# Optimization experiments

Measured on AMD Instinct MI355X. Metric: run time of the kernel, lower is better.

The kernel has to match this reference:

```python
import jax, jax.numpy as jnp
import numpy as np

D_MODEL = 1024
NUM_HEADS = 16
HEAD_DIM = D_MODEL // NUM_HEADS
SCALE = HEAD_DIM ** -0.5


def setup_inputs() -> dict:
    key = jax.random.key(0)
    ks = jax.random.split(key, 5)
    x = jax.random.normal(ks[0], (2, 2048, D_MODEL), dtype=jnp.float32)
    w_qkv = jax.random.normal(ks[1], (D_MODEL, 3 * D_MODEL), dtype=jnp.float32) * (D_MODEL ** -0.5)
    b_qkv = jnp.zeros((3 * D_MODEL,), dtype=jnp.float32)
    w_out = jax.random.normal(ks[2], (D_MODEL, D_MODEL), dtype=jnp.float32) * (D_MODEL ** -0.5)
    b_out = jnp.zeros((D_MODEL,), dtype=jnp.float32)
    return {"x": x, "w_qkv": w_qkv, "b_qkv": b_qkv, "w_out": w_out, "b_out": b_out}


def reference(x, w_qkv, b_qkv, w_out, b_out):
    b, t, _ = x.shape
    qkv = x @ w_qkv + b_qkv  # [b, t, 3*d_model]
    q, k, v = jnp.split(qkv, 3, axis=-1)
    # b t (h d) -> b h t d
    def heads(z):
        return z.reshape(b, t, NUM_HEADS, HEAD_DIM).transpose(0, 2, 1, 3)
    q, k, v = heads(q), heads(k), heads(v)
    scores = jnp.einsum('bhtd,bhsd->bhts', q, k) * SCALE
    causal = jnp.tril(jnp.ones((t, t), dtype=bool))  # True = keep
    scores = jnp.where(causal, scores, -jnp.inf)
    weights = jax.nn.softmax(scores, axis=-1)
    out = jnp.einsum('bhts,bhsd->bhtd', weights, v)
    out = out.transpose(0, 2, 1, 3).reshape(b, t, D_MODEL)  # b h t d -> b t (h d)
    return out @ w_out + b_out
```

## Files before the change

kernel.cpp:

```cpp
#include <hip/hip_runtime.h>

#define D_MODEL 1024
#define NHEADS 16
#define HDIM 64
#define SEQ 2048
#define BATCH 2
#define M_TOTAL (BATCH * SEQ)
#define N_QKV (3 * D_MODEL)

typedef __attribute__((ext_vector_type(8))) short short8;
typedef __attribute__((ext_vector_type(4))) float f32x4;
typedef __attribute__((ext_vector_type(4))) unsigned short u16x4;
typedef unsigned short u16;

__device__ __forceinline__ u16 f2bf(float f) {
  union { float f; unsigned u; } v; v.f = f;
  unsigned u = v.u + 0x7fffu + ((v.u >> 16) & 1u);
  return (u16)(u >> 16);
}

__device__ __forceinline__ unsigned pack_bf16(float lo, float hi) {
  return (unsigned)f2bf(lo) | ((unsigned)f2bf(hi) << 16);
}

__device__ __forceinline__ void gload_lds16(const void* g, void* l) {
  __builtin_amdgcn_global_load_lds(
      (__attribute__((address_space(1))) void*)(g),
      (__attribute__((address_space(3))) void*)(l),
      16, 0, 0);
}

__global__ void k_cvt_bf16(const float* __restrict__ src, u16* __restrict__ dst, int n4) {
  int i = blockIdx.x * blockDim.x + threadIdx.x;
  if (i >= n4) return;
  const float4 v = reinterpret_cast<const float4*>(src)[i];
  u16x4 o;
  o.x = f2bf(v.x); o.y = f2bf(v.y); o.z = f2bf(v.z); o.w = f2bf(v.w);
  reinterpret_cast<u16x4*>(dst)[i] = o;
}

__global__ void k_transpose_bf16(const float* __restrict__ src, u16* __restrict__ dst, int R, int C) {
  __shared__ float tile[32][33];
  const int bx = blockIdx.x * 32;
  const int by = blockIdx.y * 32;
  const int tx = threadIdx.x, ty = threadIdx.y;
  #pragma unroll
  for (int i = ty; i < 32; i += 8) tile[i][tx] = src[(size_t)(by + i) * C + bx + tx];
  __syncthreads();
  #pragma unroll
  for (int i = ty; i < 32; i += 8) dst[(size_t)(bx + i) * R + by + tx] = f2bf(tile[tx][i]);
}

template <int K, int BM, int BN, int WC>
__device__ __forceinline__ void gemm_core(const u16* __restrict__ A, const u16* __restrict__ Bt,
                                          int m0, int n0, u16* As, u16* Bs, f32x4* acc) {
  constexpr int WR = 4 / WC;
  constexpr int MI = BM / WR / 16;
  constexpr int NI = BN / WC / 16;
  const int tid = threadIdx.x;
  const int lane = tid & 63;
  const int lr = lane & 15, lg = lane >> 4;
  const int wid = tid >> 6;
  const int wr = (wid / WC) * (BM / WR);
  const int wc = (wid % WC) * (BN / WC);
  for (int kt = 0; kt < K; kt += 32) {
    #pragma unroll
    for (int r = 0; r < BM / 64; ++r) {
      const int off = r * 4096 + tid * 16;
      const int row = off >> 6, colb = off & 63;
      gload_lds16((const char*)A + ((size_t)(m0 + row) * K + kt) * 2 + colb, (char*)As + off);
    }
    #pragma unroll
    for (int r = 0; r < BN / 64; ++r) {
      const int off = r * 4096 + tid * 16;
      const int row = off >> 6, colb = off & 63;
      gload_lds16((const char*)Bt + ((size_t)(n0 + row) * K + kt) * 2 + colb, (char*)Bs + off);
    }
    __syncthreads();
    short8 a[MI], b[NI];
    #pragma unroll
    for (int i = 0; i < MI; ++i) a[i] = *(const short8*)&As[(wr + i * 16 + lr) * 32 + lg * 8];
    #pragma unroll
    for (int i = 0; i < NI; ++i) b[i] = *(const short8*)&Bs[(wc + i * 16 + lr) * 32 + lg * 8];
    #pragma unroll
    for (int mi = 0; mi < MI; ++mi)
      #pragma unroll
      for (int ni = 0; ni < NI; ++ni)
        acc[mi * NI + ni] = __builtin_amdgcn_mfma_f32_16x16x32_bf16(a[mi], b[ni], acc[mi * NI + ni], 0, 0, 0);
    __syncthreads();
  }
}

__global__ __launch_bounds__(256) void k_gemm_qkv(const u16* __restrict__ A, const u16* __restrict__ Bt,
                                                  const float* __restrict__ bias,
                                                  u16* __restrict__ qb, u16* __restrict__ kb,
                                                  u16* __restrict__ vb) {
  __shared__ u16 As[128 * 32];
  __shared__ u16 Bs[128 * 32];
  f32x4 acc[16] = {};
  const int m0 = blockIdx.x * 128, n0 = blockIdx.y * 128;
  gemm_core<D_MODEL, 128, 128, 2>(A, Bt, m0, n0, As, Bs, acc);
  const int lane = threadIdx.x & 63, lr = lane & 15, lg = lane >> 4;
  const int wid = threadIdx.x >> 6;
  const int wr = (wid >> 1) * 64, wc = (wid & 1) * 64;
  #pragma unroll
  for (int ni = 0; ni < 4; ++ni) {
    const int col = n0 + wc + ni * 16 + lr;
    const float bv = bias[col];
    const int which = col >> 10;
    const int h = (col >> 6) & 15;
    const int d = col & 63;
    #pragma unroll
    for (int mi = 0; mi < 4; ++mi) {
      #pragma unroll
      for (int j = 0; j < 4; ++j) {
        const int rw = m0 + wr + mi * 16 + lg * 4 + j;
        const int bb = rw >> 11, t = rw & (SEQ - 1);
        const u16 val = f2bf(acc[mi * 4 + ni][j] + bv);
        const int bh = bb * NHEADS + h;
        if (which == 0)      qb[((size_t)bh * SEQ + t) * HDIM + d] = val;
        else if (which == 1) kb[((size_t)bh * SEQ + t) * HDIM + d] = val;
        else                 vb[((size_t)bh * HDIM + d) * SEQ + t] = val;
      }
    }
  }
}

__global__ __launch_bounds__(256) void k_gemm_out(const u16* __restrict__ A, const u16* __restrict__ Bt,
                                                  const float* __restrict__ bias,
                                                  float* __restrict__ out) {
  __shared__ u16 As[64 * 32];
  __shared__ u16 Bs[128 * 32];
  f32x4 acc[8] = {};
  const int m0 = blockIdx.x * 64, n0 = blockIdx.y * 128;
  gemm_core<D_MODEL, 64, 128, 4>(A, Bt, m0, n0, As, Bs, acc);
  const int lane = threadIdx.x & 63, lr = lane & 15, lg = lane >> 4;
  const int wid = threadIdx.x >> 6;
  const int wc = wid * 32;
  #pragma unroll
  for (int ni = 0; ni < 2; ++ni) {
    const int col = n0 + wc + ni * 16 + lr;
    const float bv = bias[col];
    #pragma unroll
    for (int mi = 0; mi < 4; ++mi) {
      #pragma unroll
      for (int j = 0; j < 4; ++j) {
        const int rw = m0 + mi * 16 + lg * 4 + j;
        out[(size_t)rw * D_MODEL + col] = acc[mi * 2 + ni][j] + bv;
      }
    }
  }
}

__global__ __launch_bounds__(256) void k_attn(const u16* __restrict__ qb, const u16* __restrict__ kb,
                                              const u16* __restrict__ vb, u16* __restrict__ attn) {
  __shared__ u16 Ks[2][64 * 64];
  __shared__ u16 Vs[2][64 * 64];
  __shared__ u16 Pl[4][16 * 64];
  const int tid = threadIdx.x, lane = tid & 63, wid = tid >> 6;
  const int lr = lane & 15, lg = lane >> 4;
  const int lin = blockIdx.x;
  const int r = lin >> 8, c = lin & 255;
  const int a = c >> 3;
  const int qrank = (r & 1) ? a : (31 - a);
  const int bh = (c & 7) | (r << 3);
  const int b = bh >> 4, h = bh & 15;
  const int q0 = qrank * 64;
  const int qw = q0 + wid * 16;
  const u16* Q = qb + (size_t)bh * SEQ * HDIM;
  const u16* Kp = kb + (size_t)bh * SEQ * HDIM;
  const u16* Vp = vb + (size_t)bh * HDIM * SEQ;
  u16* Pw = &Pl[wid][0];

  auto stage = [&](int buf, int st_) {
    const int s0_ = st_ * 64;
    #pragma unroll
    for (int rr = 0; rr < 2; ++rr) {
      const int off = rr * 4096 + tid * 16;
      const int row = off >> 7;
      const int colb = (off & 127) ^ ((row & 7) << 4);
      gload_lds16((const char*)Kp + (size_t)(s0_ + row) * (HDIM * 2) + colb, (char*)&Ks[buf][0] + off);
      gload_lds16((const char*)Vp + ((size_t)row * SEQ + s0_) * 2 + colb, (char*)&Vs[buf][0] + off);
    }
  };

  short8 aq[2];
  #pragma unroll
  for (int ks = 0; ks < 2; ++ks)
    aq[ks] = *(const short8*)&Q[(size_t)(qw + lr) * HDIM + ks * 32 + lg * 8];

  short8 onesf;
  #pragma unroll
  for (int e = 0; e < 8; ++e) onesf[e] = (short)0x3F80;

  f32x4 acc[4] = {};
  f32x4 accl = {};

  const float sc = 0.125f * 1.44269504089f;
  const float FM = 12.0f;
  const int ntile = qrank + 1;

  stage(0, 0);
  __syncthreads();

  for (int st = 0; st < ntile; ++st) {
    const int s0 = st * 64;
    const int cur = st & 1;
    if (st + 1 < ntile) stage(cur ^ 1, st + 1);

    if (s0 <= qw + 15) {
      const char* Kt = (const char*)&Ks[cur][0];
      const char* Vt = (const char*)&Vs[cur][0];

      f32x4 s[4] = {};
      #pragma unroll
      for (int ks = 0; ks < 2; ++ks) {
        #pragma unroll
        for (int ni = 0; ni < 4; ++ni) {
          const int row = ni * 16 + lr;
          const short8 kf = *(const short8*)(Kt + row * 128 + ((ks * 64 + lg * 16) ^ ((row & 7) << 4)));
          s[ni] = __builtin_amdgcn_mfma_f32_16x16x32_bf16(kf, aq[ks], s[ni], 0, 0, 0);
        }
      }

      const bool need_mask = (s0 + 63 > qw);
      const int qq = qw + lr;
      #pragma unroll
      for (int ni = 0; ni < 4; ++ni)
        #pragma unroll
        for (int j = 0; j < 4; ++j) {
          float v = s[ni][j] * sc - FM;
          if (need_mask) {
            const int ss = s0 + ni * 16 + lg * 4 + j;
            v = (ss > qq) ? -1e30f : v;
          }
          s[ni][j] = exp2f(v);
        }

      #pragma unroll
      for (int ni = 0; ni < 4; ++ni) {
        uint2 w;
        w.x = pack_bf16(s[ni][0], s[ni][1]);
        w.y = pack_bf16(s[ni][2], s[ni][3]);
        const int byte = (lr * 128 + ni * 32 + lg * 8) ^ ((lr & 7) << 4);
        *(uint2*)((char*)Pw + byte) = w;
      }

      #pragma unroll
      for (int ks = 0; ks < 2; ++ks) {
        const int byte = (lr * 128 + ks * 64 + lg * 16) ^ ((lr & 7) << 4);
        const short8 pa = *(const short8*)((const char*)Pw + byte);
        accl = __builtin_amdgcn_mfma_f32_16x16x32_bf16(pa, onesf, accl, 0, 0, 0);
        #pragma unroll
        for (int ni = 0; ni < 4; ++ni) {
          const int row = ni * 16 + lr;
          const short8 vfr = *(const short8*)(Vt + row * 128 + ((ks * 64 + lg * 16) ^ ((row & 7) << 4)));
          acc[ni] = __builtin_amdgcn_mfma_f32_16x16x32_bf16(pa, vfr, acc[ni], 0, 0, 0);
        }
      }
    }

    __syncthreads();
  }

  #pragma unroll
  for (int j = 0; j < 4; ++j) {
    const float inv = 1.f / accl[j];
    const int t = qw + lg * 4 + j;
    #pragma unroll
    for (int ni = 0; ni < 4; ++ni) {
      const int col = h * HDIM + ni * 16 + lr;
      attn[((size_t)b * SEQ + t) * D_MODEL + col] = f2bf(acc[ni][j] * inv);
    }
  }
}

extern "C" void kernel_launch(void* const* d_in, const int* in_sizes, int n_in,
                              void* d_out, int out_size, void* d_ws, size_t ws_size,
                              hipStream_t stream) {
  const float* x     = (const float*)d_in[0];
  const float* w_qkv = (const float*)d_in[1];
  const float* b_qkv = (const float*)d_in[2];
  const float* w_out = (const float*)d_in[3];
  const float* b_out = (const float*)d_in[4];
  float* out = (float*)d_out;

  char* ws = (char*)d_ws;
  u16* xb    = (u16*)(ws);
  u16* wqkvT = (u16*)(ws + ((size_t)8 << 20));
  u16* woutT = (u16*)(ws + ((size_t)14 << 20));
  u16* qbuf  = (u16*)(ws + ((size_t)16 << 20));
  u16* kbuf  = (u16*)(ws + ((size_t)24 << 20));
  u16* vbuf  = (u16*)(ws + ((size_t)32 << 20));
  u16* attn  = (u16*)(ws + ((size_t)40 << 20));

  k_cvt_bf16<<<(M_TOTAL * D_MODEL / 4 + 255) / 256, 256, 0, stream>>>(x, xb, M_TOTAL * D_MODEL / 4);
  k_transpose_bf16<<<dim3(N_QKV / 32, D_MODEL / 32), dim3(32, 8), 0, stream>>>(w_qkv, wqkvT, D_MODEL, N_QKV);
  k_transpose_bf16<<<dim3(D_MODEL / 32, D_MODEL / 32), dim3(32, 8), 0, stream>>>(w_out, woutT, D_MODEL, D_MODEL);
  k_gemm_qkv<<<dim3(M_TOTAL / 128, N_QKV / 128), 256, 0, stream>>>(xb, wqkvT, b_qkv, qbuf, kbuf, vbuf);
  k_attn<<<1024, 256, 0, stream>>>(qbuf, kbuf, vbuf, attn);
  k_gemm_out<<<dim3(M_TOTAL / 64, D_MODEL / 128), 256, 0, stream>>>(attn, woutT, b_out, out);
}
```

Measured before the change: 199.5 us.

## Split long causal attention rows into two KV chunks with combine kernel

Query tiles 16-31 now have their KV range split into two blocks (tiles 0-15 and 16-QR), giving 1536 attention blocks of more even length. Each block writes unnormalized bf16 outputs and row sums to workspace, and a new combine kernel adds the partials and normalizes. It also drops the per-wave skip of fully masked tiles. The aim is better load balance and a shorter tail on the longest blocks, at the cost of an extra launch, extra memory traffic and an extra bf16 rounding of the partial outputs.

```diff
diff --git a/kernel.cpp b/kernel.cpp
--- a/kernel.cpp
+++ b/kernel.cpp
@@ -17,6 +17,11 @@
   union { float f; unsigned u; } v; v.f = f;
   unsigned u = v.u + 0x7fffu + ((v.u >> 16) & 1u);
   return (u16)(u >> 16);
+}
+
+__device__ __forceinline__ float bf2f(u16 x) {
+  union { unsigned u; float f; } v; v.u = ((unsigned)x) << 16;
+  return v.f;
 }
 
 __device__ __forceinline__ unsigned pack_bf16(float lo, float hi) {
@@ -153,19 +158,28 @@
 }
 
 __global__ __launch_bounds__(256) void k_attn(const u16* __restrict__ qb, const u16* __restrict__ kb,
-                                              const u16* __restrict__ vb, u16* __restrict__ attn) {
+                                              const u16* __restrict__ vb, u16* __restrict__ attnraw,
+                                              u16* __restrict__ part1, float* __restrict__ l0,
+                                              float* __restrict__ l1) {
   __shared__ u16 Ks[2][64 * 64];
   __shared__ u16 Vs[2][64 * 64];
   __shared__ u16 Pl[4][16 * 64];
   const int tid = threadIdx.x, lane = tid & 63, wid = tid >> 6;
   const int lr = lane & 15, lg = lane >> 4;
   const int lin = blockIdx.x;
-  const int r = lin >> 8, c = lin & 255;
-  const int a = c >> 3;
-  const int qrank = (r & 1) ? a : (31 - a);
-  const int bh = (c & 7) | (r << 3);
+  const int bh = lin / 48;
+  const int cc = lin - bh * 48;
+  int QR, t0, t1, chunk;
+  if (cc < 16) { QR = cc; chunk = 0; t0 = 0; t1 = QR + 1; }
+  else {
+    const int e = cc - 16;
+    QR = 16 + (e >> 1);
+    chunk = e & 1;
+    t0 = chunk ? 16 : 0;
+    t1 = chunk ? (QR + 1) : 16;
+  }
   const int b = bh >> 4, h = bh & 15;
-  const int q0 = qrank * 64;
+  const int q0 = QR * 64;
   const int qw = q0 + wid * 16;
   const u16* Q = qb + (size_t)bh * SEQ * HDIM;
   const u16* Kp = kb + (size_t)bh * SEQ * HDIM;
@@ -198,81 +212,106 @@
 
   const float sc = 0.125f * 1.44269504089f;
   const float FM = 12.0f;
-  const int ntile = qrank + 1;
-
-  stage(0, 0);
+
+  stage(0, t0);
   __syncthreads();
 
-  for (int st = 0; st < ntile; ++st) {
+  for (int st = t0; st < t1; ++st) {
     const int s0 = st * 64;
-    const int cur = st & 1;
-    if (st + 1 < ntile) stage(cur ^ 1, st + 1);
-
-    if (s0 <= qw + 15) {
-      const char* Kt = (const char*)&Ks[cur][0];
-      const char* Vt = (const char*)&Vs[cur][0];
-
-      f32x4 s[4] = {};
-      #pragma unroll
-      for (int ks = 0; ks < 2; ++ks) {
-        #pragma unroll
-        for (int ni = 0; ni < 4; ++ni) {
-          const int row = ni * 16 + lr;
-          const short8 kf = *(const short8*)(Kt + row * 128 + ((ks * 64 + lg * 16) ^ ((row & 7) << 4)));
-          s[ni] = __builtin_amdgcn_mfma_f32_16x16x32_bf16(kf, aq[ks], s[ni], 0, 0, 0);
+    const int cur = (st - t0) & 1;
+    if (st + 1 < t1) stage(cur ^ 1, st + 1);
+
+    const char* Kt = (const char*)&Ks[cur][0];
+    const char* Vt = (const char*)&Vs[cur][0];
+
+    f32x4 s[4] = {};
+    #pragma unroll
+    for (int ks = 0; ks < 2; ++ks) {
+      #pragma unroll
+      for (int ni = 0; ni < 4; ++ni) {
+        const int row = ni * 16 + lr;
+        const short8 kf = *(const short8*)(Kt + row * 128 + ((ks * 64 + lg * 16) ^ ((row & 7) << 4)));
+        s[ni] = __builtin_amdgcn_mfma_f32_16x16x32_bf16(kf, aq[ks], s[ni], 0, 0, 0);
+      }
+    }
+
+    const bool need_mask = (st == QR);
+    const int qq = qw + lr;
+    #pragma unroll
+    for (int ni = 0; ni < 4; ++ni)
+      #pragma unroll
+      for (int j = 0; j < 4; ++j) {
+        float v = s[ni][j] * sc - FM;
+        if (need_mask) {
+          const int ss = s0 + ni * 16 + lg * 4 + j;
+          v = (ss > qq) ? -1e30f : v;
         }
-      }
-
-      const bool need_mask = (s0 + 63 > qw);
-      const int qq = qw + lr;
-      #pragma unroll
-      for (int ni = 0; ni < 4; ++ni)
-        #pragma unroll
-        for (int j = 0; j < 4; ++j) {
-          float v = s[ni][j] * sc - FM;
-          if (need_mask) {
-            const int ss = s0 + ni * 16 + lg * 4 + j;
-            v = (ss > qq) ? -1e30f : v;
-          }
-          s[ni][j] = exp2f(v);
-        }
-
+        s[ni][j] = exp2f(v);
+      }
+
+    #pragma unroll
+    for (int ni = 0; ni < 4; ++ni) {
+      uint2 w;
+      w.x = pack_bf16(s[ni][0], s[ni][1]);
+      w.y = pack_bf16(s[ni][2], s[ni][3]);
+      const int byte = (lr * 128 + ni * 32 + lg * 8) ^ ((lr & 7) << 4);
+      *(uint2*)((char*)Pw + byte) = w;
+    }
+
+    #pragma unroll
+    for (int ks = 0; ks < 2; ++ks) {
+      const int byte = (lr * 128 + ks * 64 + lg * 16) ^ ((lr & 7) << 4);
+      const short8 pa = *(const short8*)((const char*)Pw + byte);
+      accl = __builtin_amdgcn_mfma_f32_16x16x32_bf16(pa, onesf, accl, 0, 0, 0);
       #pragma unroll
       for (int ni = 0; ni < 4; ++ni) {
-        uint2 w;
-        w.x = pack_bf16(s[ni][0], s[ni][1]);
-        w.y = pack_bf16(s[ni][2], s[ni][3]);
-        const int byte = (lr * 128 + ni * 32 + lg * 8) ^ ((lr & 7) << 4);
-        *(uint2*)((char*)Pw + byte) = w;
-      }
-
-      #pragma unroll
-      for (int ks = 0; ks < 2; ++ks) {
-        const int byte = (lr * 128 + ks * 64 + lg * 16) ^ ((lr & 7) << 4);
-        const short8 pa = *(const short8*)((const char*)Pw + byte);
-        accl = __builtin_amdgcn_mfma_f32_16x16x32_bf16(pa, onesf, accl, 0, 0, 0);
-        #pragma unroll
-        for (int ni = 0; ni < 4; ++ni) {
-          const int row = ni * 16 + lr;
-          const short8 vfr = *(const short8*)(Vt + row * 128 + ((ks * 64 + lg * 16) ^ ((row & 7) << 4)));
-          acc[ni] = __builtin_amdgcn_mfma_f32_16x16x32_bf16(pa, vfr, acc[ni], 0, 0, 0);
-        }
+        const int row = ni * 16 + lr;
+        const short8 vfr = *(const short8*)(Vt + row * 128 + ((ks * 64 + lg * 16) ^ ((row & 7) << 4)));
+        acc[ni] = __builtin_amdgcn_mfma_f32_16x16x32_bf16(pa, vfr, acc[ni], 0, 0, 0);
       }
     }
 
     __syncthreads();
   }
 
+  u16* od = chunk ? part1 : attnraw;
+  float* ld = chunk ? l1 : l0;
   #pragma unroll
   for (int j = 0; j < 4; ++j) {
-    const float inv = 1.f / accl[j];
     const int t = qw + lg * 4 + j;
+    if (lr == 0) ld[bh * SEQ + t] = accl[j];
     #pragma unroll
     for (int ni = 0; ni < 4; ++ni) {
       const int col = h * HDIM + ni * 16 + lr;
-      attn[((size_t)b * SEQ + t) * D_MODEL + col] = f2bf(acc[ni][j] * inv);
-    }
-  }
+      od[((size_t)b * SEQ + t) * D_MODEL + col] = f2bf(acc[ni][j]);
+    }
+  }
+}
+
+__global__ __launch_bounds__(256) void k_combine(u16* __restrict__ attnb, const u16* __restrict__ part1,
+                                                 const float* __restrict__ l0, const float* __restrict__ l1) {
+  const int i8 = blockIdx.x * 256 + threadIdx.x;
+  const size_t base = (size_t)i8 * 8;
+  const int row = i8 >> 7;
+  const int t = row & (SEQ - 1), bb = row >> 11;
+  const int h = (i8 & 127) >> 3;
+  const int bh = bb * NHEADS + h;
+  float l = l0[bh * SEQ + t];
+  short8 v = *(const short8*)(attnb + base);
+  float o[8];
+  #pragma unroll
+  for (int e = 0; e < 8; ++e) o[e] = bf2f((u16)v[e]);
+  if (t >= 1024) {
+    l += l1[bh * SEQ + t];
+    const short8 p = *(const short8*)(part1 + base);
+    #pragma unroll
+    for (int e = 0; e < 8; ++e) o[e] += bf2f((u16)p[e]);
+  }
+  const float inv = 1.f / l;
+  short8 w;
+  #pragma unroll
+  for (int e = 0; e < 8; ++e) w[e] = (short)f2bf(o[e] * inv);
+  *(short8*)(attnb + base) = w;
 }
 
 extern "C" void kernel_launch(void* const* d_in, const int* in_sizes, int n_in,
@@ -293,11 +332,15 @@
   u16* kbuf  = (u16*)(ws + ((size_t)24 << 20));
   u16* vbuf  = (u16*)(ws + ((size_t)32 << 20));
   u16* attn  = (u16*)(ws + ((size_t)40 << 20));
+  u16*   part1 = xb;
+  float* l0    = (float*)(ws + ((size_t)8 << 20));
+  float* l1    = l0 + 32 * SEQ;
 
   k_cvt_bf16<<<(M_TOTAL * D_MODEL / 4 + 255) / 256, 256, 0, stream>>>(x, xb, M_TOTAL * D_MODEL / 4);
   k_transpose_bf16<<<dim3(N_QKV / 32, D_MODEL / 32), dim3(32, 8), 0, stream>>>(w_qkv, wqkvT, D_MODEL, N_QKV);
   k_transpose_bf16<<<dim3(D_MODEL / 32, D_MODEL / 32), dim3(32, 8), 0, stream>>>(w_out, woutT, D_MODEL, D_MODEL);
   k_gemm_qkv<<<dim3(M_TOTAL / 128, N_QKV / 128), 256, 0, stream>>>(xb, wqkvT, b_qkv, qbuf, kbuf, vbuf);
-  k_attn<<<1024, 256, 0, stream>>>(qbuf, kbuf, vbuf, attn);
+  k_attn<<<32 * 48, 256, 0, stream>>>(qbuf, kbuf, vbuf, attn, part1, l0, l1);
+  k_combine<<<M_TOTAL * D_MODEL / 8 / 256, 256, 0, stream>>>(attn, part1, l0, l1);
   k_gemm_out<<<dim3(M_TOTAL / 64, D_MODEL / 128), 256, 0, stream>>>(attn, woutT, b_out, out);
 }
```

Measured after the change: 212.0 us. +6.3%, slower.
